# Optimization experiments

Measured on AMD Instinct MI355X. Metric: run time of the kernel, lower is better.

## Reference

```python
import jax, jax.numpy as jnp
import numpy as np

IN_FEATURES = 4096
OUT_FEATURES = 12288
GROUP_SIZE = 128
NUM_GROUPS = (IN_FEATURES + GROUP_SIZE - 1) // GROUP_SIZE  # 32
PADDED_IN = NUM_GROUPS * GROUP_SIZE  # 4096 (no padding needed here)


def setup_inputs() -> dict:
    key = jax.random.key(0)
    kx, kq, ks, kb = jax.random.split(key, 4)
    x = jax.random.normal(kx, (8, 32, IN_FEATURES), dtype=jnp.float16)
    # int8 quantized weight in [-128, 127]
    weight_q = jax.random.randint(kq, (OUT_FEATURES, PADDED_IN), -128, 128, dtype=jnp.int32).astype(jnp.int8)
    # positive per-(row, group) symmetric scales, fp16, clamped >= 1e-8 as in load_from_float_weight
    scales = (jax.random.uniform(ks, (OUT_FEATURES, NUM_GROUPS), dtype=jnp.float32) * 0.01 + 1e-4).astype(jnp.float16)
    bias = (jax.random.normal(kb, (OUT_FEATURES,), dtype=jnp.float32) * 0.02).astype(jnp.float16)
    return {"x": x, "scales": scales, "bias": bias, "weight_q": weight_q}


def reference(x, scales, bias, weight_q):
    # Dequantize: [O, P] int8 -> [O, G, gs] fp16, scaled per (row, group)
    compute_dtype = jnp.float16
    q3 = weight_q.astype(compute_dtype).reshape(OUT_FEATURES, NUM_GROUPS, GROUP_SIZE)
    w = (q3 * scales.astype(compute_dtype)[:, :, None]).reshape(OUT_FEATURES, PADDED_IN)[:, :IN_FEATURES]
    # F.linear: y = x @ w.T + b
    out = jnp.einsum('bsi,oi->bso', x, w) + bias.astype(compute_dtype)
    return out
```

## Files before the change

### kernel.cpp

```cpp
#include <hip/hip_runtime.h>

typedef _Float16 h16x8 __attribute__((ext_vector_type(8)));
typedef _Float16 h16x4 __attribute__((ext_vector_type(4)));
typedef _Float16 h16x2 __attribute__((ext_vector_type(2)));
typedef float    f32x4 __attribute__((ext_vector_type(4)));

#define NDIM   12288
#define KDIM   4096
#define MDIM   256
#define N_TILE 48
#define NT     32

__global__ __launch_bounds__(256) void cvt_x_kernel(const float* __restrict__ x,
                                                    _Float16* __restrict__ xf) {
    int i = blockIdx.x * 256 + threadIdx.x;
    f32x4 v = *(const f32x4*)(x + (size_t)i * 4);
    h16x4 h;
    h[0] = (_Float16)v[0]; h[1] = (_Float16)v[1];
    h[2] = (_Float16)v[2]; h[3] = (_Float16)v[3];
    *(h16x4*)(xf + (size_t)i * 4) = h;
}

template<int USE_F16X>
__global__ __launch_bounds__(1024, 4) void qlin_kernel(
    const float*    __restrict__ xf32,
    const _Float16* __restrict__ xf16,
    const float*    __restrict__ scales,
    const float*    __restrict__ bias,
    const int*      __restrict__ wq,
    float*          __restrict__ out)
{
    __shared__ char  wl[2][N_TILE * 256];
    __shared__ float sc[N_TILE * 32];

    const int tid  = threadIdx.x;
    const int lane = tid & 63;
    const int wave = tid >> 6;
    const int n0   = blockIdx.x * N_TILE;

    for (int j = tid; j < N_TILE * 32; j += 1024)
        sc[j] = scales[(size_t)(n0 + (j >> 5)) * 32 + (j & 31)];

    const int2* wb0 = (const int2*)wq + (size_t)(n0 + wave     ) * 2048 + lane;
    const int2* wb1 = (const int2*)wq + (size_t)(n0 + wave + 16) * 2048 + lane;
    const int2* wb2 = (const int2*)wq + (size_t)(n0 + wave + 32) * 2048 + lane;
    const int xors = (wave & 7) << 4;
    const int wo0  = (wave     ) * 256 + ((lane * 4) ^ xors);
    const int wo1  = (wave + 16) * 256 + ((lane * 4) ^ xors);
    const int wo2  = (wave + 32) * 256 + ((lane * 4) ^ xors);

    auto cw = [&](char* buf, int g, int2 a, int2 b, int2 c) {
        float s0 = sc[(wave     ) * 32 + g];
        float s1 = sc[(wave + 16) * 32 + g];
        float s2 = sc[(wave + 32) * 32 + g];
        h16x2 h;
        h[0] = (_Float16)((float)a.x * s0); h[1] = (_Float16)((float)a.y * s0);
        *(h16x2*)(buf + wo0) = h;
        h[0] = (_Float16)((float)b.x * s1); h[1] = (_Float16)((float)b.y * s1);
        *(h16x2*)(buf + wo1) = h;
        h[0] = (_Float16)((float)c.x * s2); h[1] = (_Float16)((float)c.y * s2);
        *(h16x2*)(buf + wo2) = h;
    };

    const int arow = lane & 15;
    const int g16  = lane >> 4;
    const int xorv = (arow & 7) << 4;
    const size_t aidx0 = (size_t)(wave * 16 + arow) * KDIM + g16 * 8;

    auto load_a = [&](size_t idx) -> h16x8 {
        if constexpr (USE_F16X) {
            return *(const h16x8*)(xf16 + idx);
        } else {
            f32x4 u0 = *(const f32x4*)(xf32 + idx);
            f32x4 u1 = *(const f32x4*)(xf32 + idx + 4);
            h16x8 a;
            a[0] = (_Float16)u0[0]; a[1] = (_Float16)u0[1];
            a[2] = (_Float16)u0[2]; a[3] = (_Float16)u0[3];
            a[4] = (_Float16)u1[0]; a[5] = (_Float16)u1[1];
            a[6] = (_Float16)u1[2]; a[7] = (_Float16)u1[3];
            return a;
        }
    };

    f32x4 acc0 = {0.f, 0.f, 0.f, 0.f}, acc1 = acc0, acc2 = acc0;

    __syncthreads();

    int2 q00 = wb0[0],   q01 = wb1[0],   q02 = wb2[0];
    int2 qa0 = wb0[64],  qa1 = wb1[64],  qa2 = wb2[64];
    int2 qb0 = wb0[128], qb1 = wb1[128], qb2 = wb2[128];
    cw(&wl[0][0], 0, q00, q01, q02);
    asm volatile("s_waitcnt lgkmcnt(0)" ::: "memory");
    __builtin_amdgcn_s_barrier();

    for (int t = 0; t < NT; ++t) {
        char* bufr = &wl[t & 1][0];
        char* bufw = &wl[(t + 1) & 1][0];

        const size_t ab = aidx0 + (size_t)t * 128;
        h16x8 a0 = load_a(ab);
        h16x8 a1 = load_a(ab + 32);
        h16x8 a2 = load_a(ab + 64);
        h16x8 a3 = load_a(ab + 96);
        const int tn = (t + 3 < NT) ? (t + 3) * 64 : (NT - 1) * 64;
        int2 qn0 = wb0[tn], qn1 = wb1[tn], qn2 = wb2[tn];

        #pragma unroll
        for (int kk = 0; kk < 4; ++kk) {
            const int bo = (kk * 64 + g16 * 16) ^ xorv;
            h16x8 b0 = *(const h16x8*)(bufr + (     arow) * 256 + bo);
            h16x8 b1 = *(const h16x8*)(bufr + (16 + arow) * 256 + bo);
            h16x8 b2 = *(const h16x8*)(bufr + (32 + arow) * 256 + bo);
            h16x8 a  = (kk == 0) ? a0 : (kk == 1) ? a1 : (kk == 2) ? a2 : a3;
            acc0 = __builtin_amdgcn_mfma_f32_16x16x32_f16(a, b0, acc0, 0, 0, 0);
            acc1 = __builtin_amdgcn_mfma_f32_16x16x32_f16(a, b1, acc1, 0, 0, 0);
            acc2 = __builtin_amdgcn_mfma_f32_16x16x32_f16(a, b2, acc2, 0, 0, 0);
        }

        if (t + 1 < NT) {
            cw(bufw, t + 1, qa0, qa1, qa2);
            asm volatile("s_waitcnt lgkmcnt(0)" ::: "memory");
            __builtin_amdgcn_s_barrier();
        }
        qa0 = qb0; qa1 = qb1; qa2 = qb2;
        qb0 = qn0; qb1 = qn1; qb2 = qn2;
    }

    float bv0 = bias[n0 +      arow];
    float bv1 = bias[n0 + 16 + arow];
    float bv2 = bias[n0 + 32 + arow];
    #pragma unroll
    for (int r = 0; r < 4; ++r) {
        int m = wave * 16 + g16 * 4 + r;
        float* op = out + (size_t)m * NDIM + n0 + arow;
        op[0]  = acc0[r] + bv0;
        op[16] = acc1[r] + bv1;
        op[32] = acc2[r] + bv2;
    }
}

extern "C" void kernel_launch(void* const* d_in, const int* in_sizes, int n_in,
                              void* d_out, int out_size, void* d_ws, size_t ws_size,
                              hipStream_t stream) {
    const float* x      = (const float*)d_in[0];
    const float* scales = (const float*)d_in[1];
    const float* bias   = (const float*)d_in[2];
    const int*   wq     = (const int*)d_in[3];
    float*       out    = (float*)d_out;

    const size_t xf_bytes = (size_t)MDIM * KDIM * sizeof(_Float16);
    if (ws_size >= xf_bytes) {
        _Float16* xf = (_Float16*)d_ws;
        cvt_x_kernel<<<dim3(MDIM * KDIM / 1024), dim3(256), 0, stream>>>(x, xf);
        qlin_kernel<1><<<dim3(NDIM / N_TILE), dim3(1024), 0, stream>>>(x, xf, scales, bias, wq, out);
    } else {
        qlin_kernel<0><<<dim3(NDIM / N_TILE), dim3(1024), 0, stream>>>(x, nullptr, scales, bias, wq, out);
    }
}
```

Measured before the change: 315.6 us.

## Repack int32 weights into int8 tiles before the quantized GEMM

```diff
diff --git a/kernel.cpp b/kernel.cpp
--- a/kernel.cpp
+++ b/kernel.cpp
@@ -2,7 +2,6 @@
 
 typedef _Float16 h16x8 __attribute__((ext_vector_type(8)));
 typedef _Float16 h16x4 __attribute__((ext_vector_type(4)));
-typedef _Float16 h16x2 __attribute__((ext_vector_type(2)));
 typedef float    f32x4 __attribute__((ext_vector_type(4)));
 
 #define NDIM   12288
@@ -10,6 +9,9 @@
 #define MDIM   256
 #define N_TILE 48
 #define NT     32
+#define TILE_BYTES 6144
+#define XF_BYTES    ((size_t)MDIM * KDIM * 2)
+#define TILES_BYTES ((size_t)256 * 32 * TILE_BYTES)
 
 __global__ __launch_bounds__(256) void cvt_x_kernel(const float* __restrict__ x,
                                                     _Float16* __restrict__ xf) {
@@ -21,14 +23,29 @@
     *(h16x4*)(xf + (size_t)i * 4) = h;
 }
 
-template<int USE_F16X>
-__global__ __launch_bounds__(1024, 4) void qlin_kernel(
-    const float*    __restrict__ xf32,
-    const _Float16* __restrict__ xf16,
-    const float*    __restrict__ scales,
-    const float*    __restrict__ bias,
-    const int*      __restrict__ wq,
-    float*          __restrict__ out)
+__global__ __launch_bounds__(1024) void repack_kernel(const int* __restrict__ wq,
+                                                      unsigned char* __restrict__ tiles) {
+    const int G = blockIdx.x * 1024 + threadIdx.x;
+    const int n    = G >> 8;
+    const int koff = (G & 255) << 4;
+    const int4* src = (const int4*)(wq + (size_t)n * KDIM + koff);
+    int4 v0 = src[0], v1 = src[1], v2 = src[2], v3 = src[3];
+    uint4 P;
+    P.x = (v0.x & 255) | ((v0.y & 255) << 8) | ((v0.z & 255) << 16) | ((v0.w & 255) << 24);
+    P.y = (v1.x & 255) | ((v1.y & 255) << 8) | ((v1.z & 255) << 16) | ((v1.w & 255) << 24);
+    P.z = (v2.x & 255) | ((v2.y & 255) << 8) | ((v2.z & 255) << 16) | ((v2.w & 255) << 24);
+    P.w = (v3.x & 255) | ((v3.y & 255) << 8) | ((v3.z & 255) << 16) | ((v3.w & 255) << 24);
+    const int t = koff >> 7, kb = koff & 127;
+    const int blk = n / 48, row = n - blk * 48;
+    *(uint4*)(tiles + (size_t)(blk * 32 + t) * TILE_BYTES + row * 128 + kb) = P;
+}
+
+__global__ __launch_bounds__(1024, 4) void qlin_tiles(
+    const _Float16*      __restrict__ xf16,
+    const float*         __restrict__ scales,
+    const float*         __restrict__ bias,
+    const unsigned char* __restrict__ tiles,
+    float*               __restrict__ out)
 {
     __shared__ char  wl[2][N_TILE * 256];
     __shared__ float sc[N_TILE * 32];
@@ -41,25 +58,31 @@
     for (int j = tid; j < N_TILE * 32; j += 1024)
         sc[j] = scales[(size_t)(n0 + (j >> 5)) * 32 + (j & 31)];
 
-    const int2* wb0 = (const int2*)wq + (size_t)(n0 + wave     ) * 2048 + lane;
-    const int2* wb1 = (const int2*)wq + (size_t)(n0 + wave + 16) * 2048 + lane;
-    const int2* wb2 = (const int2*)wq + (size_t)(n0 + wave + 32) * 2048 + lane;
-    const int xors = (wave & 7) << 4;
-    const int wo0  = (wave     ) * 256 + ((lane * 4) ^ xors);
-    const int wo1  = (wave + 16) * 256 + ((lane * 4) ^ xors);
-    const int wo2  = (wave + 32) * 256 + ((lane * 4) ^ xors);
-
-    auto cw = [&](char* buf, int g, int2 a, int2 b, int2 c) {
-        float s0 = sc[(wave     ) * 32 + g];
-        float s1 = sc[(wave + 16) * 32 + g];
-        float s2 = sc[(wave + 32) * 32 + g];
-        h16x2 h;
-        h[0] = (_Float16)((float)a.x * s0); h[1] = (_Float16)((float)a.y * s0);
-        *(h16x2*)(buf + wo0) = h;
-        h[0] = (_Float16)((float)b.x * s1); h[1] = (_Float16)((float)b.y * s1);
-        *(h16x2*)(buf + wo1) = h;
-        h[0] = (_Float16)((float)c.x * s2); h[1] = (_Float16)((float)c.y * s2);
-        *(h16x2*)(buf + wo2) = h;
+    const int srow = tid >> 4;
+    const int skb  = (tid & 15) * 8;
+    const bool do_stage = tid < N_TILE * 16;
+    const unsigned char* tb = tiles + (size_t)blockIdx.x * 32 * TILE_BYTES
+                                    + srow * 128 + skb;
+    const int wdst = srow * 256 + ((skb * 2) ^ ((srow & 7) << 4));
+
+    auto ldq = [&](int t) -> int2 {
+        return do_stage ? *(const int2*)(tb + (size_t)t * TILE_BYTES) : int2{0, 0};
+    };
+    auto stage = [&](int buf, int t, int2 q) {
+        if (do_stage) {
+            float s = sc[srow * 32 + t];
+            int a = q.x, b = q.y;
+            h16x8 h;
+            h[0] = (_Float16)((float)((a << 24) >> 24) * s);
+            h[1] = (_Float16)((float)((a << 16) >> 24) * s);
+            h[2] = (_Float16)((float)((a <<  8) >> 24) * s);
+            h[3] = (_Float16)((float)( a        >> 24) * s);
+            h[4] = (_Float16)((float)((b << 24) >> 24) * s);
+            h[5] = (_Float16)((float)((b << 16) >> 24) * s);
+            h[6] = (_Float16)((float)((b <<  8) >> 24) * s);
+            h[7] = (_Float16)((float)( b        >> 24) * s);
+            *(h16x8*)(&wl[buf][wdst]) = h;
+        }
     };
 
     const int arow = lane & 15;
@@ -67,43 +90,25 @@
     const int xorv = (arow & 7) << 4;
     const size_t aidx0 = (size_t)(wave * 16 + arow) * KDIM + g16 * 8;
 
-    auto load_a = [&](size_t idx) -> h16x8 {
-        if constexpr (USE_F16X) {
-            return *(const h16x8*)(xf16 + idx);
-        } else {
-            f32x4 u0 = *(const f32x4*)(xf32 + idx);
-            f32x4 u1 = *(const f32x4*)(xf32 + idx + 4);
-            h16x8 a;
-            a[0] = (_Float16)u0[0]; a[1] = (_Float16)u0[1];
-            a[2] = (_Float16)u0[2]; a[3] = (_Float16)u0[3];
-            a[4] = (_Float16)u1[0]; a[5] = (_Float16)u1[1];
-            a[6] = (_Float16)u1[2]; a[7] = (_Float16)u1[3];
-            return a;
-        }
-    };
-
     f32x4 acc0 = {0.f, 0.f, 0.f, 0.f}, acc1 = acc0, acc2 = acc0;
 
     __syncthreads();
 
-    int2 q00 = wb0[0],   q01 = wb1[0],   q02 = wb2[0];
-    int2 qa0 = wb0[64],  qa1 = wb1[64],  qa2 = wb2[64];
-    int2 qb0 = wb0[128], qb1 = wb1[128], qb2 = wb2[128];
-    cw(&wl[0][0], 0, q00, q01, q02);
+    int2 q0 = ldq(0);
+    stage(0, 0, q0);
+    int2 qa = ldq(1), qb = ldq(2);
     asm volatile("s_waitcnt lgkmcnt(0)" ::: "memory");
     __builtin_amdgcn_s_barrier();
 
     for (int t = 0; t < NT; ++t) {
-        char* bufr = &wl[t & 1][0];
-        char* bufw = &wl[(t + 1) & 1][0];
+        const char* bufr = &wl[t & 1][0];
 
         const size_t ab = aidx0 + (size_t)t * 128;
-        h16x8 a0 = load_a(ab);
-        h16x8 a1 = load_a(ab + 32);
-        h16x8 a2 = load_a(ab + 64);
-        h16x8 a3 = load_a(ab + 96);
-        const int tn = (t + 3 < NT) ? (t + 3) * 64 : (NT - 1) * 64;
-        int2 qn0 = wb0[tn], qn1 = wb1[tn], qn2 = wb2[tn];
+        h16x8 a0 = *(const h16x8*)(xf16 + ab);
+        h16x8 a1 = *(const h16x8*)(xf16 + ab + 32);
+        h16x8 a2 = *(const h16x8*)(xf16 + ab + 64);
+        h16x8 a3 = *(const h16x8*)(xf16 + ab + 96);
+        int2 qn = ldq(t + 3 < NT ? t + 3 : NT - 1);
 
         #pragma unroll
         for (int kk = 0; kk < 4; ++kk) {
@@ -118,12 +123,11 @@
         }
 
         if (t + 1 < NT) {
-            cw(bufw, t + 1, qa0, qa1, qa2);
+            stage((t + 1) & 1, t + 1, qa);
             asm volatile("s_waitcnt lgkmcnt(0)" ::: "memory");
             __builtin_amdgcn_s_barrier();
         }
-        qa0 = qb0; qa1 = qb1; qa2 = qb2;
-        qb0 = qn0; qb1 = qn1; qb2 = qn2;
+        qa = qb; qb = qn;
     }
 
     float bv0 = bias[n0 +      arow];
@@ -139,6 +143,85 @@
     }
 }
 
+__global__ __launch_bounds__(1024, 4) void qlin_direct(
+    const float* __restrict__ xf32, const float* __restrict__ scales,
+    const float* __restrict__ bias, const int* __restrict__ wq,
+    float* __restrict__ out)
+{
+    __shared__ char  wl[2][N_TILE * 256];
+    __shared__ float sc[N_TILE * 32];
+    const int tid = threadIdx.x, lane = tid & 63, wave = tid >> 6;
+    const int n0 = blockIdx.x * N_TILE;
+    for (int j = tid; j < N_TILE * 32; j += 1024)
+        sc[j] = scales[(size_t)(n0 + (j >> 5)) * 32 + (j & 31)];
+    typedef _Float16 h16x2 __attribute__((ext_vector_type(2)));
+    const int2* wb0 = (const int2*)wq + (size_t)(n0 + wave     ) * 2048 + lane;
+    const int2* wb1 = (const int2*)wq + (size_t)(n0 + wave + 16) * 2048 + lane;
+    const int2* wb2 = (const int2*)wq + (size_t)(n0 + wave + 32) * 2048 + lane;
+    const int xors = (wave & 7) << 4;
+    const int wo0 = (wave     ) * 256 + ((lane * 4) ^ xors);
+    const int wo1 = (wave + 16) * 256 + ((lane * 4) ^ xors);
+    const int wo2 = (wave + 32) * 256 + ((lane * 4) ^ xors);
+    auto cw = [&](char* buf, int g, int2 a, int2 b, int2 c) {
+        float s0 = sc[(wave)*32+g], s1 = sc[(wave+16)*32+g], s2 = sc[(wave+32)*32+g];
+        h16x2 h;
+        h[0]=(_Float16)((float)a.x*s0); h[1]=(_Float16)((float)a.y*s0); *(h16x2*)(buf+wo0)=h;
+        h[0]=(_Float16)((float)b.x*s1); h[1]=(_Float16)((float)b.y*s1); *(h16x2*)(buf+wo1)=h;
+        h[0]=(_Float16)((float)c.x*s2); h[1]=(_Float16)((float)c.y*s2); *(h16x2*)(buf+wo2)=h;
+    };
+    const int arow = lane & 15, g16 = lane >> 4;
+    const int xorv = (arow & 7) << 4;
+    const size_t aidx0 = (size_t)(wave * 16 + arow) * KDIM + g16 * 8;
+    auto load_a = [&](size_t idx) -> h16x8 {
+        f32x4 u0 = *(const f32x4*)(xf32 + idx);
+        f32x4 u1 = *(const f32x4*)(xf32 + idx + 4);
+        h16x8 a;
+        a[0]=(_Float16)u0[0]; a[1]=(_Float16)u0[1]; a[2]=(_Float16)u0[2]; a[3]=(_Float16)u0[3];
+        a[4]=(_Float16)u1[0]; a[5]=(_Float16)u1[1]; a[6]=(_Float16)u1[2]; a[7]=(_Float16)u1[3];
+        return a;
+    };
+    f32x4 acc0 = {0.f,0.f,0.f,0.f}, acc1 = acc0, acc2 = acc0;
+    __syncthreads();
+    int2 q00=wb0[0], q01=wb1[0], q02=wb2[0];
+    int2 qa0=wb0[64], qa1=wb1[64], qa2=wb2[64];
+    int2 qb0=wb0[128], qb1=wb1[128], qb2=wb2[128];
+    cw(&wl[0][0], 0, q00, q01, q02);
+    asm volatile("s_waitcnt lgkmcnt(0)" ::: "memory");
+    __builtin_amdgcn_s_barrier();
+    for (int t = 0; t < NT; ++t) {
+        char* bufr = &wl[t & 1][0];
+        char* bufw = &wl[(t + 1) & 1][0];
+        const size_t ab = aidx0 + (size_t)t * 128;
+        h16x8 a0 = load_a(ab), a1 = load_a(ab + 32), a2 = load_a(ab + 64), a3 = load_a(ab + 96);
+        const int tn = (t + 3 < NT) ? (t + 3) * 64 : (NT - 1) * 64;
+        int2 qn0 = wb0[tn], qn1 = wb1[tn], qn2 = wb2[tn];
+        #pragma unroll
+        for (int kk = 0; kk < 4; ++kk) {
+            const int bo = (kk * 64 + g16 * 16) ^ xorv;
+            h16x8 b0 = *(const h16x8*)(bufr + (     arow) * 256 + bo);
+            h16x8 b1 = *(const h16x8*)(bufr + (16 + arow) * 256 + bo);
+            h16x8 b2 = *(const h16x8*)(bufr + (32 + arow) * 256 + bo);
+            h16x8 a  = (kk == 0) ? a0 : (kk == 1) ? a1 : (kk == 2) ? a2 : a3;
+            acc0 = __builtin_amdgcn_mfma_f32_16x16x32_f16(a, b0, acc0, 0, 0, 0);
+            acc1 = __builtin_amdgcn_mfma_f32_16x16x32_f16(a, b1, acc1, 0, 0, 0);
+            acc2 = __builtin_amdgcn_mfma_f32_16x16x32_f16(a, b2, acc2, 0, 0, 0);
+        }
+        if (t + 1 < NT) {
+            cw(bufw, t + 1, qa0, qa1, qa2);
+            asm volatile("s_waitcnt lgkmcnt(0)" ::: "memory");
+            __builtin_amdgcn_s_barrier();
+        }
+        qa0=qb0; qa1=qb1; qa2=qb2; qb0=qn0; qb1=qn1; qb2=qn2;
+    }
+    float bv0 = bias[n0 + arow], bv1 = bias[n0 + 16 + arow], bv2 = bias[n0 + 32 + arow];
+    #pragma unroll
+    for (int r = 0; r < 4; ++r) {
+        int m = wave * 16 + g16 * 4 + r;
+        float* op = out + (size_t)m * NDIM + n0 + arow;
+        op[0] = acc0[r] + bv0; op[16] = acc1[r] + bv1; op[32] = acc2[r] + bv2;
+    }
+}
+
 extern "C" void kernel_launch(void* const* d_in, const int* in_sizes, int n_in,
                               void* d_out, int out_size, void* d_ws, size_t ws_size,
                               hipStream_t stream) {
@@ -148,12 +231,13 @@
     const int*   wq     = (const int*)d_in[3];
     float*       out    = (float*)d_out;
 
-    const size_t xf_bytes = (size_t)MDIM * KDIM * sizeof(_Float16);
-    if (ws_size >= xf_bytes) {
-        _Float16* xf = (_Float16*)d_ws;
+    if (ws_size >= XF_BYTES + TILES_BYTES) {
+        _Float16*      xf    = (_Float16*)d_ws;
+        unsigned char* tiles = (unsigned char*)d_ws + XF_BYTES;
         cvt_x_kernel<<<dim3(MDIM * KDIM / 1024), dim3(256), 0, stream>>>(x, xf);
-        qlin_kernel<1><<<dim3(NDIM / N_TILE), dim3(1024), 0, stream>>>(x, xf, scales, bias, wq, out);
+        repack_kernel<<<dim3(NDIM * KDIM / 16 / 1024), dim3(1024), 0, stream>>>(wq, tiles);
+        qlin_tiles<<<dim3(NDIM / N_TILE), dim3(1024), 0, stream>>>(xf, scales, bias, tiles, out);
     } else {
-        qlin_kernel<0><<<dim3(NDIM / N_TILE), dim3(1024), 0, stream>>>(x, nullptr, scales, bias, wq, out);
-    }
-}
+        qlin_direct<<<dim3(NDIM / N_TILE), dim3(1024), 0, stream>>>(x, scales, bias, wq, out);
+    }
+}
```

After: 370.1 us. 1.17x slower.
